# Kernel tuning notes

Hardware: AMD Instinct MI355X
Metric: run time of the kernel (lower is better)

## Reference

```python
import jax, jax.numpy as jnp
import numpy as np

N_NODES = 100_000
N_EDGES = 1_600_000
N_GRAPHS = 64
EPS = 1e-7  # GENConv message epsilon
D_IN, D_H, D_OUT, OUT_DIM = 128, 192, 128, 10


def _w(k, fan_in, fan_out):
    return jax.random.normal(k, (fan_in, fan_out), jnp.float32) * (1.0 / np.sqrt(fan_in))


def setup_inputs() -> dict:
    key = jax.random.key(0)
    ks = jax.random.split(key, 8)
    return {
        "x": jax.random.normal(ks[0], (N_NODES, D_IN), jnp.float32),
        "W0": _w(ks[1], D_IN, D_H), "b0": jnp.zeros((D_H,), jnp.float32),
        "W1": _w(ks[2], D_H, D_H), "b1": jnp.zeros((D_H,), jnp.float32),
        "W2": _w(ks[3], D_H, D_H), "b2": jnp.zeros((D_H,), jnp.float32),
        "W3": _w(ks[4], D_H, D_OUT), "b3": jnp.zeros((D_OUT,), jnp.float32),
        "Wfc": _w(ks[5], D_OUT, OUT_DIM), "bfc": jnp.zeros((OUT_DIM,), jnp.float32),
        "edge_index": jax.random.randint(ks[6], (2, N_EDGES), 0, N_NODES, jnp.int32),
        "batch": jnp.sort(jax.random.randint(ks[7], (N_NODES,), 0, N_GRAPHS, jnp.int32)),
    }


def _genconv(x, W, b, src, dst):
    # GENConv (num_layers=1, aggr='add'): message = relu(x_j) + eps,
    # scatter-add to dst, residual add, single Linear MLP.
    msg = jax.nn.relu(x[src]) + EPS          # [E, d]
    agg = jax.ops.segment_sum(msg, dst, num_segments=N_NODES)  # [N, d]
    return (x + agg) @ W + b


def reference(x, W0, b0, W1, b1, W2, b2, W3, b3, Wfc, bfc, edge_index, batch):
    src, dst = edge_index[0], edge_index[1]  # source_to_target flow
    for W, b in ((W0, b0), (W1, b1), (W2, b2), (W3, b3)):
        x = _genconv(x, W, b, src, dst)
    # global mean pool over graphs
    sums = jax.ops.segment_sum(x, batch, num_segments=N_GRAPHS)
    counts = jax.ops.segment_sum(jnp.ones((x.shape[0],), x.dtype), batch,
                                 num_segments=N_GRAPHS)
    pooled = sums / jnp.maximum(counts, 1.0)[:, None]  # [G, D_OUT]
    logits = pooled @ Wfc + bfc                        # [G, OUT_DIM]
    return jax.nn.log_softmax(logits, axis=1)
```

## Files before the change

### kernel.cpp

```cpp
#include <hip/hip_runtime.h>
#include <hip/hip_bf16.h>
#include <stdint.h>

constexpr int NN = 100000;
constexpr int NE = 1600000;
constexpr int NG = 64;
constexpr int S  = 192;
constexpr int NB_SCAN = 98;
constexpr unsigned int ZOFF = (unsigned int)NN * 384u;

constexpr int PREP_CONVX_BLK = 12500;
constexpr int PREP_INDEG_BLK = 1563;
constexpr int PREP_CONVW_BLK = 480;
constexpr int PREP_GRID = PREP_CONVX_BLK + PREP_INDEG_BLK + PREP_CONVW_BLK;

typedef __bf16 bf16x8 __attribute__((ext_vector_type(8)));
typedef float  f32x16 __attribute__((ext_vector_type(16)));
typedef float  f32x2  __attribute__((ext_vector_type(2)));

union U16x4 { uint4 u; bf16x8 b; };

__device__ __forceinline__ float bl(unsigned int u) { return __uint_as_float(u << 16); }
__device__ __forceinline__ float bh(unsigned int u) { return __uint_as_float(u & 0xffff0000u); }
__device__ __forceinline__ unsigned int fb(float f) {
    unsigned int u = __float_as_uint(f);
    return (u + 0x7fffu + ((u >> 16) & 1u)) >> 16;
}
__device__ __forceinline__ unsigned int prelu(unsigned int u) {
    unsigned int r;
    asm("v_pk_max_f16 %0, %1, %2" : "=v"(r) : "v"(u), "v"(0u));
    return r;
}

__global__ __launch_bounds__(256) void k_prep(const float* __restrict__ x,
                                              const int* __restrict__ ei,
                                              const float* __restrict__ W0, const float* __restrict__ W1,
                                              const float* __restrict__ W2, const float* __restrict__ W3,
                                              unsigned short* __restrict__ A_,
                                              int* __restrict__ indeg, int* __restrict__ slot,
                                              unsigned short* __restrict__ T0, unsigned short* __restrict__ T1,
                                              unsigned short* __restrict__ T2, unsigned short* __restrict__ T3) {
    const int b = blockIdx.x;
    if (b < PREP_CONVX_BLK) {
        int id = b * 256 + threadIdx.x;
        if (id < 96) ((unsigned int*)(A_ + (size_t)NN * S))[id] = 0u;
        int row = id >> 5, c4 = id & 31;
        float4 v = ((const float4*)x)[id];
        uint2 a;
        a.x = fb(v.x) | (fb(v.y) << 16);
        a.y = fb(v.z) | (fb(v.w) << 16);
        *(uint2*)(A_ + row * S + c4 * 4) = a;
    } else if (b < PREP_CONVX_BLK + PREP_INDEG_BLK) {
        int e4 = ((b - PREP_CONVX_BLK) * 256 + threadIdx.x) * 4;
        if (e4 < NE) {
            int4 d = *(const int4*)(ei + NE + e4);
            int4 sl;
            sl.x = atomicAdd(&indeg[d.x], 1);
            sl.y = atomicAdd(&indeg[d.y], 1);
            sl.z = atomicAdd(&indeg[d.z], 1);
            sl.w = atomicAdd(&indeg[d.w], 1);
            *(int4*)(slot + e4) = sl;
        }
    } else {
        int id = (b - PREP_CONVX_BLK - PREP_INDEG_BLK) * 256 + threadIdx.x;
        const float* W; unsigned short* T; int N, base;
        if      (id <  24576) { W = W0; T = T0; N = 192; base = 0;     }
        else if (id <  61440) { W = W1; T = T1; N = 192; base = 24576; }
        else if (id <  98304) { W = W2; T = T2; N = 192; base = 61440; }
        else                  { W = W3; T = T3; N = 128; base = 98304; }
        int lid = id - base;
        int ci = lid >> 3, j = lid & 7;
        int kc = ci / N, n = ci % N;
        T[lid] = (unsigned short)fb(W[(kc * 8 + j) * N + n]);
    }
}

__global__ __launch_bounds__(1024) void k_scan1(const int* __restrict__ indeg, int* __restrict__ offs,
                                                int* __restrict__ partials) {
    __shared__ int s[1024];
    int t = threadIdx.x;
    int gid = blockIdx.x * 1024 + t;
    int v = (gid < NN) ? indeg[gid] : 0;
    s[t] = v;
    __syncthreads();
    for (int d = 1; d < 1024; d <<= 1) {
        int tv = (t >= d) ? s[t - d] : 0;
        __syncthreads();
        s[t] += tv;
        __syncthreads();
    }
    if (gid < NN) offs[gid + 1] = s[t];
    if (t == 1023) partials[blockIdx.x] = s[1023];
}

__global__ __launch_bounds__(128) void k_scan2(int* __restrict__ offs, int* __restrict__ partials) {
    __shared__ int s[128];
    int t = threadIdx.x;
    int v = (t < NB_SCAN) ? partials[t] : 0;
    s[t] = v;
    __syncthreads();
    for (int d = 1; d < 128; d <<= 1) {
        int tv = (t >= d) ? s[t - d] : 0;
        __syncthreads();
        s[t] += tv;
        __syncthreads();
    }
    if (t < NB_SCAN) partials[t] = s[t] - v;
    if (t == 0) offs[0] = 0;
}

__global__ __launch_bounds__(1024) void k_scan3(int* __restrict__ offs, const int* __restrict__ partials) {
    int gid = blockIdx.x * 1024 + threadIdx.x;
    if (gid < NN) offs[gid + 1] += partials[blockIdx.x];
}

__global__ __launch_bounds__(256) void k_fill(const int* __restrict__ ei, const int* __restrict__ offs,
                                              const int* __restrict__ slot, int* __restrict__ csr) {
    int e4 = (blockIdx.x * 256 + threadIdx.x) * 4;
    if (e4 >= NE) return;
    int4 sv = *(const int4*)(ei + e4);
    int4 dv = *(const int4*)(ei + NE + e4);
    int4 sl = *(const int4*)(slot + e4);
    csr[offs[dv.x] + sl.x] = sv.x;
    csr[offs[dv.y] + sl.y] = sv.y;
    csr[offs[dv.z] + sl.z] = sv.z;
    csr[offs[dv.w] + sl.w] = sv.w;
}

__global__ __launch_bounds__(256, 8) void k_agg192(const unsigned short* __restrict__ Ain,
                                                   unsigned short* __restrict__ Yout,
                                                   const int* __restrict__ offs,
                                                   const int* __restrict__ indeg,
                                                   const int* __restrict__ csr) {
    const int w = threadIdx.x >> 6, lane = threadIdx.x & 63;
    const int i = __builtin_amdgcn_readfirstlane(blockIdx.x * 4 + w);
    const bool act = lane < 48;
    const int deg   = __builtin_amdgcn_readfirstlane(indeg[i]);
    const int start = __builtin_amdgcn_readfirstlane(offs[i]);
    const int fo = (act ? lane : 47) * 8;
    const char* Ab = (const char*)Ain;

    f32x2 A01, A23;
    {
        uint2 p = *(const uint2*)(Ab + (size_t)i * 384 + fo);
        const float ed = 1e-7f * (float)deg;
        A01 = (f32x2){bl(p.x) + ed, bh(p.x) + ed};
        A23 = (f32x2){bl(p.y) + ed, bh(p.y) + ed};
    }

    const int* ecsr = csr + start;
    for (int e = 0; e < deg; e += 16) {
        unsigned int off[16];
#pragma unroll
        for (int k = 0; k < 16; k++) {
            int v = ecsr[e + k];
            off[k] = (e + k < deg) ? (unsigned int)v * 384u : ZOFF;
        }
        uint2 p[16];
#pragma unroll
        for (int k = 0; k < 16; k++)
            p[k] = *(const uint2*)(Ab + (size_t)off[k] + fo);
#pragma unroll
        for (int k = 0; k < 16; k++) {
            unsigned int rx = prelu(p[k].x), ry = prelu(p[k].y);
            A01 += (f32x2){bl(rx), bh(rx)};
            A23 += (f32x2){bl(ry), bh(ry)};
        }
    }
    if (act) {
        uint2 o;
        o.x = fb(A01.x) | (fb(A01.y) << 16);
        o.y = fb(A23.x) | (fb(A23.y) << 16);
        *(uint2*)(Yout + (size_t)i * S + lane * 4) = o;
    }
}

__global__ __launch_bounds__(256, 8) void k_agg128(const unsigned short* __restrict__ Ain,
                                                   unsigned short* __restrict__ Yout,
                                                   const int* __restrict__ offs,
                                                   const int* __restrict__ indeg,
                                                   const int* __restrict__ csr) {
    const int w = threadIdx.x >> 6, lane = threadIdx.x & 63;
    const int i = __builtin_amdgcn_readfirstlane(blockIdx.x * 4 + w);
    const int deg   = __builtin_amdgcn_readfirstlane(indeg[i]);
    const int start = __builtin_amdgcn_readfirstlane(offs[i]);
    const int fo = lane * 4;
    const char* Ab = (const char*)Ain;

    f32x2 A01;
    {
        unsigned int p = *(const unsigned int*)(Ab + (size_t)i * 384 + fo);
        const float ed = 1e-7f * (float)deg;
        A01 = (f32x2){bl(p) + ed, bh(p) + ed};
    }

    const int* ecsr = csr + start;
    for (int e = 0; e < deg; e += 16) {
        unsigned int off[16];
#pragma unroll
        for (int k = 0; k < 16; k++) {
            int v = ecsr[e + k];
            off[k] = (e + k < deg) ? (unsigned int)v * 384u : ZOFF;
        }
        unsigned int q[16];
#pragma unroll
        for (int k = 0; k < 16; k++)
            q[k] = *(const unsigned int*)(Ab + (size_t)off[k] + fo);
#pragma unroll
        for (int k = 0; k < 16; k++) {
            unsigned int r = prelu(q[k]);
            A01 += (f32x2){bl(r), bh(r)};
        }
    }
    *(unsigned int*)(Yout + (size_t)i * S + lane * 2) =
        fb(A01.x) | (fb(A01.y) << 16);
}

template <int K, int N>
__global__ __launch_bounds__(256) void k_gemm(const unsigned short* __restrict__ Yin,
                                              const unsigned short* __restrict__ WtC,
                                              const float* __restrict__ bias,
                                              unsigned short* __restrict__ Aout) {
    static_assert(K % 16 == 0 && N % 32 == 0, "");
    const int w = threadIdx.x >> 6, lane = threadIdx.x & 63;
    const int rt = blockIdx.x * 4 + w;
    if (rt >= (NN / 32)) return;
    const int hl = lane >> 5, lr = lane & 31;
    const int row0 = rt * 32;
    f32x16 acc[N / 32];
#pragma unroll
    for (int c = 0; c < N / 32; c++)
#pragma unroll
        for (int r = 0; r < 16; r++) acc[c][r] = 0.f;

    const unsigned short* ap = Yin + (row0 + lr) * S + hl * 8;
    const uint4* b4 = (const uint4*)WtC;
#pragma unroll
    for (int ks = 0; ks < K / 16; ks++) {
        U16x4 a;
        a.u = *(const uint4*)(ap + ks * 16);
#pragma unroll
        for (int c = 0; c < N / 32; c++) {
            U16x4 b;
            b.u = b4[(ks * 2 + hl) * N + c * 32 + lr];
            acc[c] = __builtin_amdgcn_mfma_f32_32x32x16_bf16(a.b, b.b, acc[c], 0, 0, 0);
        }
    }
#pragma unroll
    for (int c = 0; c < N / 32; c++) {
        const int col = c * 32 + lr;
        const float bc = bias[col];
#pragma unroll
        for (int r = 0; r < 16; r++) {
            const int row = row0 + (r & 3) + 8 * (r >> 2) + 4 * hl;
            Aout[row * S + col] = (unsigned short)fb(acc[c][r] + bc);
        }
    }
}

__global__ __launch_bounds__(128) void k_pool(const unsigned short* __restrict__ A_, const int* __restrict__ batch,
                                              float* __restrict__ sums, float* __restrict__ cnt) {
    const int b = blockIdx.x;
    const int f = threadIdx.x;
    int n0 = b * 200;
    int n1 = min(n0 + 200, NN);
    int cur = batch[n0];
    float acc = 0.f;
    int run = 0;
    for (int n = n0; n < n1; n++) {
        int g = batch[n];
        if (g != cur) {
            atomicAdd(&sums[cur * 128 + f], acc);
            if (f == 0) atomicAdd(&cnt[cur], (float)run);
            acc = 0.f; run = 0; cur = g;
        }
        acc += __uint_as_float(((unsigned int)A_[(size_t)n * S + f]) << 16);
        run++;
    }
    atomicAdd(&sums[cur * 128 + f], acc);
    if (f == 0) atomicAdd(&cnt[cur], (float)run);
}

__global__ __launch_bounds__(64) void k_head(const float* __restrict__ sums, const float* __restrict__ cnt,
                                             const float* __restrict__ Wfc, const float* __restrict__ bfc,
                                             float* __restrict__ out) {
    __shared__ float pooled[128];
    __shared__ float lg[10];
    const int g = blockIdx.x, t = threadIdx.x;
    float inv = 1.f / fmaxf(cnt[g], 1.f);
    pooled[t]      = sums[g * 128 + t] * inv;
    pooled[t + 64] = sums[g * 128 + t + 64] * inv;
    __syncthreads();
    if (t < 10) {
        float s = bfc[t];
        for (int f = 0; f < 128; f++) s += pooled[f] * Wfc[f * 10 + t];
        lg[t] = s;
    }
    __syncthreads();
    if (t < 10) {
        float m = lg[0];
        for (int k = 1; k < 10; k++) m = fmaxf(m, lg[k]);
        float se = 0.f;
        for (int k = 0; k < 10; k++) se += expf(lg[k] - m);
        out[g * 10 + t] = lg[t] - m - logf(se);
    }
}

constexpr size_t A0_OFF     = 0;
constexpr size_t A1_OFF     = 38400384;
constexpr size_t CSR_OFF    = 76800384;
constexpr size_t OFFS_OFF   = 83200384;
constexpr size_t INDEG_OFF  = 83600512;
constexpr size_t PART_OFF   = 84000512;
constexpr size_t WT0_OFF    = 84001024;
constexpr size_t WT1_OFF    = 84050176;
constexpr size_t WT2_OFF    = 84123904;
constexpr size_t WT3_OFF    = 84197632;
constexpr size_t SUMS_OFF   = 84246784;
constexpr size_t CNT_OFF    = 84279552;

extern "C" void kernel_launch(void* const* d_in, const int* in_sizes, int n_in,
                              void* d_out, int out_size, void* d_ws, size_t ws_size,
                              hipStream_t stream) {
    const float* x   = (const float*)d_in[0];
    const float* W0  = (const float*)d_in[1];
    const float* b0  = (const float*)d_in[2];
    const float* W1  = (const float*)d_in[3];
    const float* b1  = (const float*)d_in[4];
    const float* W2  = (const float*)d_in[5];
    const float* b2  = (const float*)d_in[6];
    const float* W3  = (const float*)d_in[7];
    const float* b3  = (const float*)d_in[8];
    const float* Wfc = (const float*)d_in[9];
    const float* bfc = (const float*)d_in[10];
    const int*   ei  = (const int*)d_in[11];
    const int*   bat = (const int*)d_in[12];
    float* out = (float*)d_out;

    char* ws = (char*)d_ws;
    unsigned short* A0  = (unsigned short*)(ws + A0_OFF);
    unsigned short* A1  = (unsigned short*)(ws + A1_OFF);
    int* slot   = (int*)(ws + A1_OFF);
    int* csr    = (int*)(ws + CSR_OFF);
    int* offs   = (int*)(ws + OFFS_OFF);
    int* indeg  = (int*)(ws + INDEG_OFF);
    int* part   = (int*)(ws + PART_OFF);
    unsigned short* Wt0 = (unsigned short*)(ws + WT0_OFF);
    unsigned short* Wt1 = (unsigned short*)(ws + WT1_OFF);
    unsigned short* Wt2 = (unsigned short*)(ws + WT2_OFF);
    unsigned short* Wt3 = (unsigned short*)(ws + WT3_OFF);
    float* sums = (float*)(ws + SUMS_OFF);
    float* cnt  = (float*)(ws + CNT_OFF);

    hipMemsetAsync(ws + INDEG_OFF, 0, 400000, stream);
    hipMemsetAsync(ws + SUMS_OFF, 0, 33024, stream);

    k_prep<<<PREP_GRID, 256, 0, stream>>>(x, ei, W0, W1, W2, W3, A0, indeg, slot,
                                          Wt0, Wt1, Wt2, Wt3);

    k_scan1<<<NB_SCAN, 1024, 0, stream>>>(indeg, offs, part);
    k_scan2<<<1, 128, 0, stream>>>(offs, part);
    k_scan3<<<NB_SCAN, 1024, 0, stream>>>(offs, part);

    k_fill<<<(NE / 4 + 255) / 256, 256, 0, stream>>>(ei, offs, slot, csr);

    const int AGG_GRID  = NN / 4;
    const int GEMM_GRID = (NN / 32 + 3) / 4;

    k_agg128<<<AGG_GRID, 256, 0, stream>>>(A0, A1, offs, indeg, csr);
    k_gemm<128, 192><<<GEMM_GRID, 256, 0, stream>>>(A1, Wt0, b0, A0);
    k_agg192<<<AGG_GRID, 256, 0, stream>>>(A0, A1, offs, indeg, csr);
    k_gemm<192, 192><<<GEMM_GRID, 256, 0, stream>>>(A1, Wt1, b1, A0);
    k_agg192<<<AGG_GRID, 256, 0, stream>>>(A0, A1, offs, indeg, csr);
    k_gemm<192, 192><<<GEMM_GRID, 256, 0, stream>>>(A1, Wt2, b2, A0);
    k_agg192<<<AGG_GRID, 256, 0, stream>>>(A0, A1, offs, indeg, csr);
    k_gemm<192, 128><<<GEMM_GRID, 256, 0, stream>>>(A1, Wt3, b3, A0);

    k_pool<<<500, 128, 0, stream>>>(A0, bat, sums, cnt);
    k_head<<<NG, 64, 0, stream>>>(sums, cnt, Wfc, bfc, out);
}
```

Before: 720.6 us.

## Fold last GENConv layer through mean pool via edge-graph histogram GEMM

Measured after the change: 766.3 us. +6.4%, slower.

```diff
diff --git a/kernel.cpp b/kernel.cpp
--- a/kernel.cpp
+++ b/kernel.cpp
@@ -11,8 +11,11 @@
 
 constexpr int PREP_CONVX_BLK = 12500;
 constexpr int PREP_INDEG_BLK = 1563;
-constexpr int PREP_CONVW_BLK = 480;
+constexpr int PREP_CONVW_BLK = 384;
 constexpr int PREP_GRID = PREP_CONVX_BLK + PREP_INDEG_BLK + PREP_CONVW_BLK;
+
+constexpr int EG_BLOCKS = 391;
+constexpr int EG_JMAX = EG_BLOCKS * 256;
 
 typedef __bf16 bf16x8 __attribute__((ext_vector_type(8)));
 typedef float  f32x16 __attribute__((ext_vector_type(16)));
@@ -22,6 +25,7 @@
 
 __device__ __forceinline__ float bl(unsigned int u) { return __uint_as_float(u << 16); }
 __device__ __forceinline__ float bh(unsigned int u) { return __uint_as_float(u & 0xffff0000u); }
+__device__ __forceinline__ float b16f(unsigned short u) { return __uint_as_float(((unsigned int)u) << 16); }
 __device__ __forceinline__ unsigned int fb(float f) {
     unsigned int u = __float_as_uint(f);
     return (u + 0x7fffu + ((u >> 16) & 1u)) >> 16;
@@ -35,11 +39,11 @@
 __global__ __launch_bounds__(256) void k_prep(const float* __restrict__ x,
                                               const int* __restrict__ ei,
                                               const float* __restrict__ W0, const float* __restrict__ W1,
-                                              const float* __restrict__ W2, const float* __restrict__ W3,
+                                              const float* __restrict__ W2,
                                               unsigned short* __restrict__ A_,
                                               int* __restrict__ indeg, int* __restrict__ slot,
                                               unsigned short* __restrict__ T0, unsigned short* __restrict__ T1,
-                                              unsigned short* __restrict__ T2, unsigned short* __restrict__ T3) {
+                                              unsigned short* __restrict__ T2) {
     const int b = blockIdx.x;
     if (b < PREP_CONVX_BLK) {
         int id = b * 256 + threadIdx.x;
@@ -64,10 +68,9 @@
     } else {
         int id = (b - PREP_CONVX_BLK - PREP_INDEG_BLK) * 256 + threadIdx.x;
         const float* W; unsigned short* T; int N, base;
-        if      (id <  24576) { W = W0; T = T0; N = 192; base = 0;     }
-        else if (id <  61440) { W = W1; T = T1; N = 192; base = 24576; }
-        else if (id <  98304) { W = W2; T = T2; N = 192; base = 61440; }
-        else                  { W = W3; T = T3; N = 128; base = 98304; }
+        if      (id < 24576) { W = W0; T = T0; N = 192; base = 0;     }
+        else if (id < 61440) { W = W1; T = T1; N = 192; base = 24576; }
+        else                 { W = W2; T = T2; N = 192; base = 61440; }
         int lid = id - base;
         int ci = lid >> 3, j = lid & 7;
         int kc = ci / N, n = ci % N;
@@ -258,42 +261,142 @@
     }
 }
 
-__global__ __launch_bounds__(128) void k_pool(const unsigned short* __restrict__ A_, const int* __restrict__ batch,
-                                              float* __restrict__ sums, float* __restrict__ cnt) {
+__global__ __launch_bounds__(256) void k_hist(const int* __restrict__ ei, const int* __restrict__ bat,
+                                              unsigned int* __restrict__ hist) {
+    int e2 = (blockIdx.x * 256 + threadIdx.x) * 2;
+    if (e2 >= NE) return;
+    int2 sv = *(const int2*)(ei + e2);
+    int2 dv = *(const int2*)(ei + NE + e2);
+    int g0 = bat[dv.x], g1 = bat[dv.y];
+    atomicAdd(&hist[sv.x * 32 + (g0 >> 1)], 1u << (16 * (g0 & 1)));
+    atomicAdd(&hist[sv.y * 32 + (g1 >> 1)], 1u << (16 * (g1 & 1)));
+}
+
+__global__ __launch_bounds__(256) void k_econv(const unsigned int* __restrict__ hist,
+                                               unsigned short* __restrict__ E) {
+    int id = blockIdx.x * 256 + threadIdx.x;
+    if (id >= EG_JMAX * 32) return;
+    int j = id >> 5, gp = id & 31;
+    unsigned int h = (j < NN) ? hist[id] : 0u;
+    unsigned short c0 = (unsigned short)fb((float)(h & 0xffffu));
+    unsigned short c1 = (unsigned short)fb((float)(h >> 16));
+    size_t base = ((size_t)(j >> 3) * 64 + gp * 2) * 8 + (j & 7);
+    E[base] = c0;
+    E[base + 8] = c1;
+}
+
+__global__ __launch_bounds__(192) void k_egemm(const unsigned short* __restrict__ A0,
+                                               const unsigned short* __restrict__ E,
+                                               unsigned short* __restrict__ partials) {
+    const int wv = threadIdx.x >> 6, lane = threadIdx.x & 63;
+    const int b = blockIdx.x;
+    const int j0 = b * 256;
+    const int hl = lane >> 5, lr = lane & 31;
+    f32x16 acc[2][2];
+#pragma unroll
+    for (int m = 0; m < 2; m++)
+#pragma unroll
+        for (int n = 0; n < 2; n++)
+#pragma unroll
+            for (int r = 0; r < 16; r++) acc[m][n][r] = 0.f;
+
+    for (int kk = 0; kk < 16; kk++) {
+        const int jb8 = (j0 >> 3) + kk * 2;
+        U16x4 af[2];
+#pragma unroll
+        for (int m = 0; m < 2; m++)
+            af[m].u = *(const uint4*)(E + ((size_t)(jb8 + hl) * 64 + m * 32 + lr) * 8);
+        U16x4 bf[2];
+#pragma unroll
+        for (int n = 0; n < 2; n++) {
+            const int feat = (2 * wv + n) * 32 + lr;
+#pragma unroll
+            for (int tp = 0; tp < 4; tp++) {
+                int je = j0 + kk * 16 + hl * 8 + tp * 2;
+                int ja = min(je, NN), jb = min(je + 1, NN);
+                unsigned int u0 = A0[(size_t)ja * S + feat];
+                unsigned int u1 = A0[(size_t)jb * S + feat];
+                ((unsigned int*)&bf[n].u)[tp] = prelu(u0 | (u1 << 16));
+            }
+        }
+#pragma unroll
+        for (int m = 0; m < 2; m++)
+#pragma unroll
+            for (int n = 0; n < 2; n++)
+                acc[m][n] = __builtin_amdgcn_mfma_f32_32x32x16_bf16(af[m].b, bf[n].b, acc[m][n], 0, 0, 0);
+    }
+    unsigned short* pb = partials + (size_t)b * 12288;
+#pragma unroll
+    for (int m = 0; m < 2; m++)
+#pragma unroll
+        for (int n = 0; n < 2; n++) {
+            const int f = (2 * wv + n) * 32 + lr;
+#pragma unroll
+            for (int r = 0; r < 16; r++) {
+                const int g = m * 32 + (r & 3) + 8 * (r >> 2) + 4 * hl;
+                pb[g * 192 + f] = (unsigned short)fb(acc[m][n][r]);
+            }
+        }
+}
+
+__global__ __launch_bounds__(256) void k_reduce(const unsigned short* __restrict__ partials,
+                                                float* __restrict__ msg) {
+    int gf = blockIdx.x * 256 + threadIdx.x;
+    if (gf >= 12288) return;
+    float s = 0.f;
+    for (int p = 0; p < EG_BLOCKS; p++)
+        s += b16f(partials[(size_t)p * 12288 + gf]);
+    msg[gf] = s;
+}
+
+__global__ __launch_bounds__(192) void k_pool(const unsigned short* __restrict__ A_,
+                                              const int* __restrict__ batch,
+                                              const int* __restrict__ indeg,
+                                              float* __restrict__ sums, float* __restrict__ cnt,
+                                              float* __restrict__ degsum) {
     const int b = blockIdx.x;
     const int f = threadIdx.x;
     int n0 = b * 200;
     int n1 = min(n0 + 200, NN);
     int cur = batch[n0];
     float acc = 0.f;
-    int run = 0;
+    int run = 0, dacc = 0;
     for (int n = n0; n < n1; n++) {
         int g = batch[n];
         if (g != cur) {
-            atomicAdd(&sums[cur * 128 + f], acc);
-            if (f == 0) atomicAdd(&cnt[cur], (float)run);
-            acc = 0.f; run = 0; cur = g;
-        }
-        acc += __uint_as_float(((unsigned int)A_[(size_t)n * S + f]) << 16);
+            atomicAdd(&sums[cur * 192 + f], acc);
+            if (f == 0) { atomicAdd(&cnt[cur], (float)run); atomicAdd(&degsum[cur], (float)dacc); }
+            acc = 0.f; run = 0; dacc = 0; cur = g;
+        }
+        acc += b16f(A_[(size_t)n * S + f]);
         run++;
-    }
-    atomicAdd(&sums[cur * 128 + f], acc);
-    if (f == 0) atomicAdd(&cnt[cur], (float)run);
-}
-
-__global__ __launch_bounds__(64) void k_head(const float* __restrict__ sums, const float* __restrict__ cnt,
-                                             const float* __restrict__ Wfc, const float* __restrict__ bfc,
-                                             float* __restrict__ out) {
-    __shared__ float pooled[128];
+        if (f == 0) dacc += indeg[n];
+    }
+    atomicAdd(&sums[cur * 192 + f], acc);
+    if (f == 0) { atomicAdd(&cnt[cur], (float)run); atomicAdd(&degsum[cur], (float)dacc); }
+}
+
+__global__ __launch_bounds__(128) void k_head(const float* __restrict__ sums, const float* __restrict__ msg,
+                                              const float* __restrict__ cnt, const float* __restrict__ degsum,
+                                              const float* __restrict__ W3, const float* __restrict__ b3,
+                                              const float* __restrict__ Wfc, const float* __restrict__ bfc,
+                                              float* __restrict__ out) {
+    __shared__ float py[192];
+    __shared__ float tl[128];
     __shared__ float lg[10];
     const int g = blockIdx.x, t = threadIdx.x;
-    float inv = 1.f / fmaxf(cnt[g], 1.f);
-    pooled[t]      = sums[g * 128 + t] * inv;
-    pooled[t + 64] = sums[g * 128 + t + 64] * inv;
+    const float inv = 1.f / fmaxf(cnt[g], 1.f);
+    const float ed = 1e-7f * degsum[g];
+    for (int k = t; k < 192; k += 128)
+        py[k] = (sums[g * 192 + k] + msg[g * 192 + k] + ed) * inv;
+    __syncthreads();
+    float tf = b3[t];
+    for (int k = 0; k < 192; k++) tf += py[k] * W3[k * 128 + t];
+    tl[t] = tf;
     __syncthreads();
     if (t < 10) {
         float s = bfc[t];
-        for (int f = 0; f < 128; f++) s += pooled[f] * Wfc[f * 10 + t];
+        for (int f = 0; f < 128; f++) s += tl[f] * Wfc[f * 10 + t];
         lg[t] = s;
     }
     __syncthreads();
@@ -308,6 +411,9 @@
 
 constexpr size_t A0_OFF     = 0;
 constexpr size_t A1_OFF     = 38400384;
+constexpr size_t HIST_REL   = 0;
+constexpr size_t E_REL      = 12800000;
+constexpr size_t PARTS_REL  = 25612288;
 constexpr size_t CSR_OFF    = 76800384;
 constexpr size_t OFFS_OFF   = 83200384;
 constexpr size_t INDEG_OFF  = 83600512;
@@ -315,9 +421,10 @@
 constexpr size_t WT0_OFF    = 84001024;
 constexpr size_t WT1_OFF    = 84050176;
 constexpr size_t WT2_OFF    = 84123904;
-constexpr size_t WT3_OFF    = 84197632;
-constexpr size_t SUMS_OFF   = 84246784;
-constexpr size_t CNT_OFF    = 84279552;
+constexpr size_t SUMS_OFF   = 84197632;
+constexpr size_t CNT_OFF    = 84246784;
+constexpr size_t DEGS_OFF   = 84247040;
+constexpr size_t MSG_OFF    = 84247296;
 
 extern "C" void kernel_launch(void* const* d_in, const int* in_sizes, int n_in,
                               void* d_out, int out_size, void* d_ws, size_t ws_size,
@@ -341,6 +448,9 @@
     unsigned short* A0  = (unsigned short*)(ws + A0_OFF);
     unsigned short* A1  = (unsigned short*)(ws + A1_OFF);
     int* slot   = (int*)(ws + A1_OFF);
+    unsigned int*   hist  = (unsigned int*)(ws + A1_OFF + HIST_REL);
+    unsigned short* Ebf   = (unsigned short*)(ws + A1_OFF + E_REL);
+    unsigned short* parts = (unsigned short*)(ws + A1_OFF + PARTS_REL);
     int* csr    = (int*)(ws + CSR_OFF);
     int* offs   = (int*)(ws + OFFS_OFF);
     int* indeg  = (int*)(ws + INDEG_OFF);
@@ -348,20 +458,19 @@
     unsigned short* Wt0 = (unsigned short*)(ws + WT0_OFF);
     unsigned short* Wt1 = (unsigned short*)(ws + WT1_OFF);
     unsigned short* Wt2 = (unsigned short*)(ws + WT2_OFF);
-    unsigned short* Wt3 = (unsigned short*)(ws + WT3_OFF);
-    float* sums = (float*)(ws + SUMS_OFF);
-    float* cnt  = (float*)(ws + CNT_OFF);
+    float* sums   = (float*)(ws + SUMS_OFF);
+    float* cnt    = (float*)(ws + CNT_OFF);
+    float* degsum = (float*)(ws + DEGS_OFF);
+    float* msg    = (float*)(ws + MSG_OFF);
 
     hipMemsetAsync(ws + INDEG_OFF, 0, 400000, stream);
-    hipMemsetAsync(ws + SUMS_OFF, 0, 33024, stream);
-
-    k_prep<<<PREP_GRID, 256, 0, stream>>>(x, ei, W0, W1, W2, W3, A0, indeg, slot,
-                                          Wt0, Wt1, Wt2, Wt3);
+    hipMemsetAsync(ws + SUMS_OFF, 0, 49664, stream);
+
+    k_prep<<<PREP_GRID, 256, 0, stream>>>(x, ei, W0, W1, W2, A0, indeg, slot, Wt0, Wt1, Wt2);
 
     k_scan1<<<NB_SCAN, 1024, 0, stream>>>(indeg, offs, part);
     k_scan2<<<1, 128, 0, stream>>>(offs, part);
     k_scan3<<<NB_SCAN, 1024, 0, stream>>>(offs, part);
-
     k_fill<<<(NE / 4 + 255) / 256, 256, 0, stream>>>(ei, offs, slot, csr);
 
     const int AGG_GRID  = NN / 4;
@@ -373,9 +482,12 @@
     k_gemm<192, 192><<<GEMM_GRID, 256, 0, stream>>>(A1, Wt1, b1, A0);
     k_agg192<<<AGG_GRID, 256, 0, stream>>>(A0, A1, offs, indeg, csr);
     k_gemm<192, 192><<<GEMM_GRID, 256, 0, stream>>>(A1, Wt2, b2, A0);
-    k_agg192<<<AGG_GRID, 256, 0, stream>>>(A0, A1, offs, indeg, csr);
-    k_gemm<192, 128><<<GEMM_GRID, 256, 0, stream>>>(A1, Wt3, b3, A0);
-
-    k_pool<<<500, 128, 0, stream>>>(A0, bat, sums, cnt);
-    k_head<<<NG, 64, 0, stream>>>(sums, cnt, Wfc, bfc, out);
-}
+
+    hipMemsetAsync(ws + A1_OFF + HIST_REL, 0, 12800000, stream);
+    k_hist<<<NE / 512, 256, 0, stream>>>(ei, bat, hist);
+    k_econv<<<(EG_JMAX * 32) / 256, 256, 0, stream>>>(hist, Ebf);
+    k_egemm<<<EG_BLOCKS, 192, 0, stream>>>(A0, Ebf, parts);
+    k_reduce<<<48, 256, 0, stream>>>(parts, msg);
+    k_pool<<<500, 192, 0, stream>>>(A0, bat, indeg, sums, cnt, degsum);
+    k_head<<<NG, 128, 0, stream>>>(sums, msg, cnt, degsum, W3, b3, Wfc, bfc, out);
+}
```
